# Performance work log

Hardware: AMD Instinct MI355X
Metric: run time of the kernel (lower is better)

Reference implementation:

```python
import jax, jax.numpy as jnp
import numpy as np

B, T, D = 4, 2048, 768
H = 12
HD = D // H
WINDOW = 128

def setup_inputs() -> dict:
    key = jax.random.key(0)
    k1, k2, k3 = jax.random.split(key, 3)
    x = jax.random.normal(k1, (B, T, D), dtype=jnp.float32)
    Wqkv = jax.random.normal(k2, (D, 3 * D), dtype=jnp.float32) * 0.02
    Wout = jax.random.normal(k3, (D, D), dtype=jnp.float32) * 0.02
    return {"x": x, "Wqkv": Wqkv, "Wout": Wout}

def reference(x, Wqkv, Wout):
    Bx, Tx, Dx = x.shape
    qkv = x @ Wqkv                      # [B,T,3D]
    q, k, v = jnp.split(qkv, 3, axis=-1)
    def heads(t):
        return t.reshape(Bx, Tx, H, HD).transpose(0, 2, 1, 3)  # [B,H,T,hd]
    q, k, v = heads(q), heads(k), heads(v)
    scale = 1.0 / jnp.sqrt(jnp.float32(HD))
    scores = jnp.einsum('bhqd,bhkd->bhqk', q, k) * scale       # [B,H,T,T]
    pos = jnp.arange(Tx)
    dist = pos[None, :] - pos[:, None]                          # j - i
    blocked = (dist > 0) | (dist < -WINDOW)                     # causal band
    scores = jnp.where(blocked[None, None], -jnp.inf, scores)
    attn = jax.nn.softmax(scores, axis=-1)
    out = jnp.einsum('bhqk,bhkd->bhqd', attn, v)                # [B,H,T,hd]
    out = out.transpose(0, 2, 1, 3).reshape(Bx, Tx, Dx)
    return out @ Wout
```

## Files before the change

kernel.cpp:

```cpp
#include <hip/hip_runtime.h>
#include <hip/hip_bf16.h>
#include <stdint.h>

typedef unsigned short u16;
typedef __attribute__((ext_vector_type(8))) short short8;
typedef __attribute__((ext_vector_type(8))) __bf16 bf16x8;
typedef __attribute__((ext_vector_type(4))) float f32x4;

constexpr int Bc  = 4;
constexpr int Tc  = 2048;
constexpr int Dc  = 768;
constexpr int Hc  = 12;
constexpr int WINc = 128;

static __device__ __forceinline__ u16 f2bf(float f) {
  union { float f; uint32_t u; } v; v.f = f;
  uint32_t u = v.u;
  return (u16)((u + 0x7fffu + ((u >> 16) & 1u)) >> 16);
}

static __device__ __forceinline__ f32x4 mfma16x16x32(bf16x8 a, bf16x8 b, f32x4 c) {
  return __builtin_amdgcn_mfma_f32_16x16x32_bf16(a, b, c, 0, 0, 0);
}

#define GLOAD_LDS16(gsrc, ldst)                                                \
  __builtin_amdgcn_global_load_lds(                                            \
      (const __attribute__((address_space(1))) void*)(gsrc),                   \
      (__attribute__((address_space(3))) void*)(ldst), 16, 0, 0)

__global__ __launch_bounds__(256) void cvt_f32_to_bf16(const float* __restrict__ in,
                                                       u16* __restrict__ out) {
  const int i = blockIdx.x * 256 + threadIdx.x;
  const float4 f = ((const float4*)in)[i];
  union { u16 h[4]; uint2 u; } pk;
  pk.h[0] = f2bf(f.x); pk.h[1] = f2bf(f.y); pk.h[2] = f2bf(f.z); pk.h[3] = f2bf(f.w);
  ((uint2*)out)[i] = pk.u;
}

__global__ __launch_bounds__(256) void transpose_cvt(const float* __restrict__ W,
                                                     u16* __restrict__ WT,
                                                     int R, int C) {
  __shared__ float tile[64][65];
  const int t  = threadIdx.x;
  const int c0 = blockIdx.x * 64, r0 = blockIdx.y * 64;
#pragma unroll
  for (int i = 0; i < 16; ++i) {
    const int e = i * 256 + t;
    const int r = e >> 6, c = e & 63;
    tile[r][c] = W[(size_t)(r0 + r) * C + c0 + c];
  }
  __syncthreads();
#pragma unroll
  for (int i = 0; i < 16; ++i) {
    const int e = i * 256 + t;
    const int r = e >> 6, c = e & 63;
    WT[(size_t)(c0 + r) * R + r0 + c] = f2bf(tile[c][r]);
  }
}

template <int EPI>
__global__ __launch_bounds__(256) void gemm_bt(const u16* __restrict__ A,
                                               const u16* __restrict__ Bt,
                                               u16* __restrict__ q_ws,
                                               u16* __restrict__ k_ws,
                                               u16* __restrict__ v_ws,
                                               float* __restrict__ fout) {
  __shared__ u16 As[128][32];
  __shared__ u16 Bs[128][32];
  const int t  = threadIdx.x;
  const int w  = t >> 6, l = t & 63;
  const int lr = l & 15, lh = l >> 4;
  const int wm = w >> 1, wn = w & 1;
  const int m0 = blockIdx.y * 128, n0 = blockIdx.x * 128;

  f32x4 acc[4][4];
#pragma unroll
  for (int mi = 0; mi < 4; ++mi)
#pragma unroll
    for (int ni = 0; ni < 4; ++ni) acc[mi][ni] = f32x4{0.f, 0.f, 0.f, 0.f};

  const int srow = l >> 2;
  const int scol = (l & 3) * 8;
  const u16* aP = A  + (size_t)(m0 + w * 16 + srow) * 768 + scol;
  const u16* bP = Bt + (size_t)(n0 + w * 16 + srow) * 768 + scol;
  char* asB = (char*)As + w * 1024;
  char* bsB = (char*)Bs + w * 1024;

  for (int kt = 0; kt < 24; ++kt) {
    const int ko = kt * 32;
    __syncthreads();
    GLOAD_LDS16(aP + ko,            asB);
    GLOAD_LDS16(aP + ko + 64 * 768, asB + 4096);
    GLOAD_LDS16(bP + ko,            bsB);
    GLOAD_LDS16(bP + ko + 64 * 768, bsB + 4096);
    __syncthreads();

    bf16x8 af[4], bfr[4];
#pragma unroll
    for (int mi = 0; mi < 4; ++mi)
      af[mi] = *(const bf16x8*)&As[wm * 64 + mi * 16 + lr][lh * 8];
#pragma unroll
    for (int ni = 0; ni < 4; ++ni)
      bfr[ni] = *(const bf16x8*)&Bs[wn * 64 + ni * 16 + lr][lh * 8];
#pragma unroll
    for (int mi = 0; mi < 4; ++mi)
#pragma unroll
      for (int ni = 0; ni < 4; ++ni)
        acc[mi][ni] = mfma16x16x32(af[mi], bfr[ni], acc[mi][ni]);
  }

  if (EPI == 0) {
#pragma unroll
    for (int mi = 0; mi < 4; ++mi)
#pragma unroll
      for (int ni = 0; ni < 4; ++ni) {
        const int col   = n0 + wn * 64 + ni * 16 + lr;
        const int which = col / 768;
        const int rem   = col - which * 768;
        const int h     = rem >> 6, d = rem & 63;
        u16* dst = (which == 0) ? q_ws : ((which == 1) ? k_ws : v_ws);
#pragma unroll
        for (int r = 0; r < 4; ++r) {
          const int m  = m0 + wm * 64 + mi * 16 + lh * 4 + r;
          const int bb = m >> 11, tt = m & 2047;
          dst[(((size_t)(bb * Hc + h) * Tc + tt) << 6) + d] = f2bf(acc[mi][ni][r]);
        }
      }
  } else {
#pragma unroll
    for (int mi = 0; mi < 4; ++mi)
#pragma unroll
      for (int ni = 0; ni < 4; ++ni) {
        const int col = n0 + wn * 64 + ni * 16 + lr;
#pragma unroll
        for (int r = 0; r < 4; ++r) {
          const int m = m0 + wm * 64 + mi * 16 + lh * 4 + r;
          fout[(size_t)m * 768 + col] = acc[mi][ni][r];
        }
      }
  }
}

__global__ __launch_bounds__(256) void swa_attn(const u16* __restrict__ Q,
                                                const u16* __restrict__ Kk,
                                                const u16* __restrict__ V,
                                                u16* __restrict__ Out) {
  __shared__ u16 Qs[64][72];
  __shared__ u16 Ks[64][72];
  __shared__ u16 Vt[64][72];
  __shared__ u16 Ps[4][16][72];

  const int t  = threadIdx.x;
  const int w  = t >> 6, l = t & 63;
  const int lr = l & 15, lh = l >> 4;
  const int bh = blockIdx.y;
  const int q0 = blockIdx.x * 64;
  const size_t head_base = (size_t)bh * Tc * 64;

  {
    const int row = t >> 2, c = (t & 3) * 16;
    const short8* src = (const short8*)(Q + head_base + (size_t)(q0 + row) * 64 + c);
    *(short8*)&Qs[row][c]     = src[0];
    *(short8*)&Qs[row][c + 8] = src[1];
  }

  float m_r[4], l_r[4];
  f32x4 Oa[4];
#pragma unroll
  for (int r = 0; r < 4; ++r) { m_r[r] = -1e30f; l_r[r] = 0.f; }
#pragma unroll
  for (int n = 0; n < 4; ++n) Oa[n] = f32x4{0.f, 0.f, 0.f, 0.f};

  const int kb_lo = (q0 >= WINc) ? q0 - WINc : 0;
  for (int kb = kb_lo; kb <= q0; kb += 64) {
    __syncthreads();
    {
      const int row = t >> 2, c = (t & 3) * 16;
      const short8* ksrc = (const short8*)(Kk + head_base + (size_t)(kb + row) * 64 + c);
      *(short8*)&Ks[row][c]     = ksrc[0];
      *(short8*)&Ks[row][c + 8] = ksrc[1];
      const short8* vsrc = (const short8*)(V + head_base + (size_t)(kb + row) * 64 + c);
      short8 v0 = vsrc[0], v1 = vsrc[1];
#pragma unroll
      for (int j = 0; j < 8; ++j) {
        Vt[c + j][row]     = (u16)v0[j];
        Vt[c + 8 + j][row] = (u16)v1[j];
      }
    }
    __syncthreads();

    bf16x8 qa0 = *(const bf16x8*)&Qs[w * 16 + lr][lh * 8];
    bf16x8 qa1 = *(const bf16x8*)&Qs[w * 16 + lr][32 + lh * 8];

    f32x4 s[4];
#pragma unroll
    for (int sub = 0; sub < 4; ++sub) {
      bf16x8 kb0 = *(const bf16x8*)&Ks[sub * 16 + lr][lh * 8];
      bf16x8 kb1 = *(const bf16x8*)&Ks[sub * 16 + lr][32 + lh * 8];
      f32x4 z = f32x4{0.f, 0.f, 0.f, 0.f};
      z = mfma16x16x32(qa0, kb0, z);
      z = mfma16x16x32(qa1, kb1, z);
      s[sub] = z;
    }

    const int qbase = q0 + w * 16 + lh * 4;
#pragma unroll
    for (int sub = 0; sub < 4; ++sub) {
      const int kj = kb + sub * 16 + lr;
#pragma unroll
      for (int r = 0; r < 4; ++r) {
        const int qi = qbase + r;
        const bool ok = (kj <= qi) && (kj + WINc >= qi);
        s[sub][r] = ok ? s[sub][r] * 0.125f : -1e30f;
      }
    }

    float mt[4];
#pragma unroll
    for (int r = 0; r < 4; ++r)
      mt[r] = fmaxf(fmaxf(s[0][r], s[1][r]), fmaxf(s[2][r], s[3][r]));
#pragma unroll
    for (int msk = 1; msk < 16; msk <<= 1)
#pragma unroll
      for (int r = 0; r < 4; ++r)
        mt[r] = fmaxf(mt[r], __shfl_xor(mt[r], msk, 64));

    float al[4];
#pragma unroll
    for (int r = 0; r < 4; ++r) {
      const float mn = fmaxf(m_r[r], mt[r]);
      al[r] = __expf(m_r[r] - mn);
      m_r[r] = mn;
    }

    float rs[4] = {0.f, 0.f, 0.f, 0.f};
#pragma unroll
    for (int sub = 0; sub < 4; ++sub)
#pragma unroll
      for (int r = 0; r < 4; ++r) {
        const float p = __expf(s[sub][r] - m_r[r]);
        s[sub][r] = p;
        rs[r] += p;
      }
#pragma unroll
    for (int msk = 1; msk < 16; msk <<= 1)
#pragma unroll
      for (int r = 0; r < 4; ++r)
        rs[r] += __shfl_xor(rs[r], msk, 64);
#pragma unroll
    for (int r = 0; r < 4; ++r) l_r[r] = l_r[r] * al[r] + rs[r];

#pragma unroll
    for (int n = 0; n < 4; ++n)
#pragma unroll
      for (int r = 0; r < 4; ++r) Oa[n][r] *= al[r];

#pragma unroll
    for (int sub = 0; sub < 4; ++sub)
#pragma unroll
      for (int r = 0; r < 4; ++r)
        Ps[w][lh * 4 + r][sub * 16 + lr] = f2bf(s[sub][r]);

#pragma unroll
    for (int ks = 0; ks < 2; ++ks) {
      bf16x8 pa = *(const bf16x8*)&Ps[w][lr][ks * 32 + lh * 8];
#pragma unroll
      for (int n = 0; n < 4; ++n) {
        bf16x8 vb = *(const bf16x8*)&Vt[n * 16 + lr][ks * 32 + lh * 8];
        Oa[n] = mfma16x16x32(pa, vb, Oa[n]);
      }
    }
  }

  const int bb = bh / Hc, h = bh - bb * Hc;
#pragma unroll
  for (int n = 0; n < 4; ++n)
#pragma unroll
    for (int r = 0; r < 4; ++r) {
      const float val = Oa[n][r] / l_r[r];
      const int ti = q0 + w * 16 + lh * 4 + r;
      Out[((size_t)(bb * Tc + ti)) * 768 + h * 64 + n * 16 + lr] = f2bf(val);
    }
}

extern "C" void kernel_launch(void* const* d_in, const int* in_sizes, int n_in,
                              void* d_out, int out_size, void* d_ws, size_t ws_size,
                              hipStream_t stream) {
  (void)in_sizes; (void)n_in; (void)out_size; (void)ws_size;
  const float* x    = (const float*)d_in[0];
  const float* Wqkv = (const float*)d_in[1];
  const float* Wout = (const float*)d_in[2];
  float* out = (float*)d_out;

  u16* ws    = (u16*)d_ws;
  u16* xb    = ws;
  u16* wqkvT = xb + 6291456;
  u16* woutT = wqkvT + 1769472;
  u16* qws   = woutT + 589824;
  u16* kws   = qws + 6291456;
  u16* vws   = kws + 6291456;
  u16* aws   = xb;

  cvt_f32_to_bf16<<<6144, 256, 0, stream>>>(x, xb);
  transpose_cvt<<<dim3(36, 12), 256, 0, stream>>>(Wqkv, wqkvT, 768, 2304);
  transpose_cvt<<<dim3(12, 12), 256, 0, stream>>>(Wout, woutT, 768, 768);
  gemm_bt<0><<<dim3(18, 64), 256, 0, stream>>>(xb, wqkvT, qws, kws, vws, nullptr);
  swa_attn<<<dim3(32, 48), 256, 0, stream>>>(qws, kws, vws, aws);
  gemm_bt<1><<<dim3(6, 64), 256, 0, stream>>>(aws, woutT, nullptr, nullptr, nullptr, out);
}
```

Measured before the change: 113.6 us.

## Double-buffer GEMM LDS tiles and have QKV GEMM emit transposed V for attention

The GEMM main loop now double-buffers its shared-memory A/B tiles, prefetching the next K-slice while MFMAs run on the current one, so there is one barrier per iteration instead of two. The QKV GEMM epilogue writes V already transposed ([bh][d][t]). The attention kernel drops its shared-memory staging of Q, K and V and loads the MFMA fragments straight from global memory. Each wave now walks only the key blocks its own 16 query rows need, which removes the in-LDS V transpose and the block barriers. The trade-off is redundant global/L2 reads of K and V across the four waves and strided transposed-V stores in the GEMM epilogue.

Result: slower. 145.6 us (+28.2%).

```diff
diff --git a/kernel.cpp b/kernel.cpp
--- a/kernel.cpp
+++ b/kernel.cpp
@@ -65,8 +65,8 @@
                                                u16* __restrict__ k_ws,
                                                u16* __restrict__ v_ws,
                                                float* __restrict__ fout) {
-  __shared__ u16 As[128][32];
-  __shared__ u16 Bs[128][32];
+  __shared__ u16 As[2][128][32];
+  __shared__ u16 Bs[2][128][32];
   const int t  = threadIdx.x;
   const int w  = t >> 6, l = t & 63;
   const int lr = l & 15, lh = l >> 4;
@@ -86,22 +86,45 @@
   char* asB = (char*)As + w * 1024;
   char* bsB = (char*)Bs + w * 1024;
 
-  for (int kt = 0; kt < 24; ++kt) {
-    const int ko = kt * 32;
+  GLOAD_LDS16(aP,            asB);
+  GLOAD_LDS16(aP + 64 * 768, asB + 4096);
+  GLOAD_LDS16(bP,            bsB);
+  GLOAD_LDS16(bP + 64 * 768, bsB + 4096);
+  __syncthreads();
+
+  int p = 0;
+  for (int kt = 0; kt < 23; ++kt) {
+    {
+      const int ko = (kt + 1) * 32;
+      const int bo = (p ^ 1) * 8192;
+      GLOAD_LDS16(aP + ko,            asB + bo);
+      GLOAD_LDS16(aP + ko + 64 * 768, asB + bo + 4096);
+      GLOAD_LDS16(bP + ko,            bsB + bo);
+      GLOAD_LDS16(bP + ko + 64 * 768, bsB + bo + 4096);
+    }
+    bf16x8 af[4], bfr[4];
+#pragma unroll
+    for (int mi = 0; mi < 4; ++mi)
+      af[mi] = *(const bf16x8*)&As[p][wm * 64 + mi * 16 + lr][lh * 8];
+#pragma unroll
+    for (int ni = 0; ni < 4; ++ni)
+      bfr[ni] = *(const bf16x8*)&Bs[p][wn * 64 + ni * 16 + lr][lh * 8];
+#pragma unroll
+    for (int mi = 0; mi < 4; ++mi)
+#pragma unroll
+      for (int ni = 0; ni < 4; ++ni)
+        acc[mi][ni] = mfma16x16x32(af[mi], bfr[ni], acc[mi][ni]);
     __syncthreads();
-    GLOAD_LDS16(aP + ko,            asB);
-    GLOAD_LDS16(aP + ko + 64 * 768, asB + 4096);
-    GLOAD_LDS16(bP + ko,            bsB);
-    GLOAD_LDS16(bP + ko + 64 * 768, bsB + 4096);
-    __syncthreads();
-
+    p ^= 1;
+  }
+  {
     bf16x8 af[4], bfr[4];
 #pragma unroll
     for (int mi = 0; mi < 4; ++mi)
-      af[mi] = *(const bf16x8*)&As[wm * 64 + mi * 16 + lr][lh * 8];
+      af[mi] = *(const bf16x8*)&As[p][wm * 64 + mi * 16 + lr][lh * 8];
 #pragma unroll
     for (int ni = 0; ni < 4; ++ni)
-      bfr[ni] = *(const bf16x8*)&Bs[wn * 64 + ni * 16 + lr][lh * 8];
+      bfr[ni] = *(const bf16x8*)&Bs[p][wn * 64 + ni * 16 + lr][lh * 8];
 #pragma unroll
     for (int mi = 0; mi < 4; ++mi)
 #pragma unroll
@@ -118,12 +141,17 @@
         const int which = col / 768;
         const int rem   = col - which * 768;
         const int h     = rem >> 6, d = rem & 63;
-        u16* dst = (which == 0) ? q_ws : ((which == 1) ? k_ws : v_ws);
 #pragma unroll
         for (int r = 0; r < 4; ++r) {
           const int m  = m0 + wm * 64 + mi * 16 + lh * 4 + r;
           const int bb = m >> 11, tt = m & 2047;
-          dst[(((size_t)(bb * Hc + h) * Tc + tt) << 6) + d] = f2bf(acc[mi][ni][r]);
+          const u16 val = f2bf(acc[mi][ni][r]);
+          if (which == 0)
+            q_ws[(((size_t)(bb * Hc + h) * Tc + tt) << 6) + d] = val;
+          else if (which == 1)
+            k_ws[(((size_t)(bb * Hc + h) * Tc + tt) << 6) + d] = val;
+          else
+            v_ws[(((size_t)((bb * Hc + h) * 64 + d)) << 11) + tt] = val;
         }
       }
   } else {
@@ -143,26 +171,20 @@
 
 __global__ __launch_bounds__(256) void swa_attn(const u16* __restrict__ Q,
                                                 const u16* __restrict__ Kk,
-                                                const u16* __restrict__ V,
+                                                const u16* __restrict__ Vt,
                                                 u16* __restrict__ Out) {
-  __shared__ u16 Qs[64][72];
-  __shared__ u16 Ks[64][72];
-  __shared__ u16 Vt[64][72];
   __shared__ u16 Ps[4][16][72];
 
   const int t  = threadIdx.x;
   const int w  = t >> 6, l = t & 63;
   const int lr = l & 15, lh = l >> 4;
   const int bh = blockIdx.y;
-  const int q0 = blockIdx.x * 64;
-  const size_t head_base = (size_t)bh * Tc * 64;
-
-  {
-    const int row = t >> 2, c = (t & 3) * 16;
-    const short8* src = (const short8*)(Q + head_base + (size_t)(q0 + row) * 64 + c);
-    *(short8*)&Qs[row][c]     = src[0];
-    *(short8*)&Qs[row][c + 8] = src[1];
-  }
+  const int q0 = blockIdx.x * 64 + w * 16;
+  const size_t hb  = (size_t)bh * (Tc * 64);
+  const size_t hbv = (size_t)bh * (64 * Tc);
+
+  const bf16x8 qa0 = *(const bf16x8*)(Q + hb + (size_t)(q0 + lr) * 64 + lh * 8);
+  const bf16x8 qa1 = *(const bf16x8*)(Q + hb + (size_t)(q0 + lr) * 64 + 32 + lh * 8);
 
   float m_r[4], l_r[4];
   f32x4 Oa[4];
@@ -171,39 +193,30 @@
 #pragma unroll
   for (int n = 0; n < 4; ++n) Oa[n] = f32x4{0.f, 0.f, 0.f, 0.f};
 
-  const int kb_lo = (q0 >= WINc) ? q0 - WINc : 0;
-  for (int kb = kb_lo; kb <= q0; kb += 64) {
-    __syncthreads();
-    {
-      const int row = t >> 2, c = (t & 3) * 16;
-      const short8* ksrc = (const short8*)(Kk + head_base + (size_t)(kb + row) * 64 + c);
-      *(short8*)&Ks[row][c]     = ksrc[0];
-      *(short8*)&Ks[row][c + 8] = ksrc[1];
-      const short8* vsrc = (const short8*)(V + head_base + (size_t)(kb + row) * 64 + c);
-      short8 v0 = vsrc[0], v1 = vsrc[1];
-#pragma unroll
-      for (int j = 0; j < 8; ++j) {
-        Vt[c + j][row]     = (u16)v0[j];
-        Vt[c + 8 + j][row] = (u16)v1[j];
-      }
-    }
-    __syncthreads();
-
-    bf16x8 qa0 = *(const bf16x8*)&Qs[w * 16 + lr][lh * 8];
-    bf16x8 qa1 = *(const bf16x8*)&Qs[w * 16 + lr][32 + lh * 8];
-
+  const int kb_lo = (q0 >= WINc) ? ((q0 - WINc) & ~63) : 0;
+  const int kb_hi = q0 & ~63;
+  for (int kb = kb_lo; kb <= kb_hi; kb += 64) {
     f32x4 s[4];
 #pragma unroll
     for (int sub = 0; sub < 4; ++sub) {
-      bf16x8 kb0 = *(const bf16x8*)&Ks[sub * 16 + lr][lh * 8];
-      bf16x8 kb1 = *(const bf16x8*)&Ks[sub * 16 + lr][32 + lh * 8];
+      const u16* kr = Kk + hb + (size_t)(kb + sub * 16 + lr) * 64;
+      const bf16x8 kf0 = *(const bf16x8*)(kr + lh * 8);
+      const bf16x8 kf1 = *(const bf16x8*)(kr + 32 + lh * 8);
       f32x4 z = f32x4{0.f, 0.f, 0.f, 0.f};
-      z = mfma16x16x32(qa0, kb0, z);
-      z = mfma16x16x32(qa1, kb1, z);
+      z = mfma16x16x32(qa0, kf0, z);
+      z = mfma16x16x32(qa1, kf1, z);
       s[sub] = z;
     }
 
-    const int qbase = q0 + w * 16 + lh * 4;
+    bf16x8 vf[2][4];
+#pragma unroll
+    for (int ks = 0; ks < 2; ++ks)
+#pragma unroll
+      for (int ni = 0; ni < 4; ++ni)
+        vf[ks][ni] = *(const bf16x8*)(Vt + hbv + (size_t)(ni * 16 + lr) * Tc
+                                      + kb + ks * 32 + lh * 8);
+
+    const int qbase = q0 + lh * 4;
 #pragma unroll
     for (int sub = 0; sub < 4; ++sub) {
       const int kj = kb + sub * 16 + lr;
@@ -238,9 +251,9 @@
     for (int sub = 0; sub < 4; ++sub)
 #pragma unroll
       for (int r = 0; r < 4; ++r) {
-        const float p = __expf(s[sub][r] - m_r[r]);
-        s[sub][r] = p;
-        rs[r] += p;
+        const float pv = __expf(s[sub][r] - m_r[r]);
+        s[sub][r] = pv;
+        rs[r] += pv;
       }
 #pragma unroll
     for (int msk = 1; msk < 16; msk <<= 1)
@@ -263,24 +276,23 @@
 
 #pragma unroll
     for (int ks = 0; ks < 2; ++ks) {
-      bf16x8 pa = *(const bf16x8*)&Ps[w][lr][ks * 32 + lh * 8];
-#pragma unroll
-      for (int n = 0; n < 4; ++n) {
-        bf16x8 vb = *(const bf16x8*)&Vt[n * 16 + lr][ks * 32 + lh * 8];
-        Oa[n] = mfma16x16x32(pa, vb, Oa[n]);
-      }
+      const bf16x8 pa = *(const bf16x8*)&Ps[w][lr][ks * 32 + lh * 8];
+#pragma unroll
+      for (int ni = 0; ni < 4; ++ni)
+        Oa[ni] = mfma16x16x32(pa, vf[ks][ni], Oa[ni]);
     }
   }
 
   const int bb = bh / Hc, h = bh - bb * Hc;
 #pragma unroll
-  for (int n = 0; n < 4; ++n)
-#pragma unroll
-    for (int r = 0; r < 4; ++r) {
-      const float val = Oa[n][r] / l_r[r];
-      const int ti = q0 + w * 16 + lh * 4 + r;
-      Out[((size_t)(bb * Tc + ti)) * 768 + h * 64 + n * 16 + lr] = f2bf(val);
-    }
+  for (int r = 0; r < 4; ++r) {
+    const float inv = 1.f / l_r[r];
+    const int ti = q0 + lh * 4 + r;
+#pragma unroll
+    for (int ni = 0; ni < 4; ++ni)
+      Out[((size_t)(bb * Tc + ti)) * 768 + h * 64 + ni * 16 + lr] =
+          f2bf(Oa[ni][r] * inv);
+  }
 }
 
 extern "C" void kernel_launch(void* const* d_in, const int* in_sizes, int n_in,
@@ -298,13 +310,13 @@
   u16* woutT = wqkvT + 1769472;
   u16* qws   = woutT + 589824;
   u16* kws   = qws + 6291456;
-  u16* vws   = kws + 6291456;
+  u16* vtws  = kws + 6291456;
   u16* aws   = xb;
 
   cvt_f32_to_bf16<<<6144, 256, 0, stream>>>(x, xb);
   transpose_cvt<<<dim3(36, 12), 256, 0, stream>>>(Wqkv, wqkvT, 768, 2304);
   transpose_cvt<<<dim3(12, 12), 256, 0, stream>>>(Wout, woutT, 768, 768);
-  gemm_bt<0><<<dim3(18, 64), 256, 0, stream>>>(xb, wqkvT, qws, kws, vws, nullptr);
-  swa_attn<<<dim3(32, 48), 256, 0, stream>>>(qws, kws, vws, aws);
+  gemm_bt<0><<<dim3(18, 64), 256, 0, stream>>>(xb, wqkvT, qws, kws, vtws, nullptr);
+  swa_attn<<<dim3(32, 48), 256, 0, stream>>>(qws, kws, vtws, aws);
   gemm_bt<1><<<dim3(6, 64), 256, 0, stream>>>(aws, woutT, nullptr, nullptr, nullptr, out);
 }
```
